# Performance work log

Hardware: AMD Instinct MI355X
Metric: run time of the kernel (lower is better)

The kernel has to match this reference:

```python
import jax, jax.numpy as jnp
import numpy as np

B, S, D = 8, 4096, 1024
C = D // 4          # bottleneck width (downsize=4)
P = 64              # num_prompt_tokens
EPS = 1e-5          # BatchNorm1d eps


def setup_inputs() -> dict:
    key = jax.random.key(0)
    ks = jax.random.split(key, 5)
    return {
        "hidden_states": jax.random.normal(ks[0], (B, S, D), dtype=jnp.float32),
        "W_down": jax.random.normal(ks[1], (C, D), dtype=jnp.float32) / np.sqrt(D),
        "b_down": jax.random.normal(ks[2], (C,), dtype=jnp.float32) * 0.02,
        "gamma": jnp.ones((C,), dtype=jnp.float32),
        "beta": jnp.zeros((C,), dtype=jnp.float32),
        "W_up": jax.random.normal(ks[3], (D, C), dtype=jnp.float32) / np.sqrt(C),
        "b_up": jax.random.normal(ks[4], (D,), dtype=jnp.float32) * 0.02,
    }


def reference(hidden_states, W_down, b_down, gamma, beta, W_up, b_up):
    # proj_down: [B,S,D] -> [B,S,C]
    h = jnp.einsum("bsd,cd->bsc", hidden_states, W_down) + b_down
    b, s, c = h.shape
    win = s // P  # S is a multiple of P, so AdaptiveMaxPool1d == windowed max
    # adaptive max pool over the sequence dim: [B,S,C] -> [B,P,C]
    h = h.reshape(b, P, win, c).max(axis=2)
    h = jax.nn.relu(h)
    # BatchNorm1d over channel dim (training mode: batch stats over B and P)
    mean = h.mean(axis=(0, 1))
    var = ((h - mean) ** 2).mean(axis=(0, 1))  # biased variance, as in BN
    h = (h - mean) * jax.lax.rsqrt(var + EPS) * gamma + beta
    # proj_up: [B,P,C] -> [B,P,D]
    return jnp.einsum("bpc,dc->bpd", h, W_up) + b_up
```

## Files before the change

kernel.cpp:

```cpp
#include <hip/hip_runtime.h>

#define D_  1024
#define C_  256
#define NBP 512

using bf16x8 = __attribute__((ext_vector_type(8))) __bf16;
using f32x4  = __attribute__((ext_vector_type(4))) float;

__device__ __forceinline__ unsigned short f2bf(float x) {
  unsigned int u = __float_as_uint(x);
  u += 0x7fffu + ((u >> 16) & 1u);
  return (unsigned short)(u >> 16);
}

typedef __attribute__((address_space(1))) const void* gas_t;
typedef __attribute__((address_space(3))) void* las_t;
__device__ __forceinline__ void dma16(const void* g, void* l) {
  __builtin_amdgcn_global_load_lds((gas_t)g, (las_t)l, 16, 0, 0);
}

__global__ void k_prep(const float* __restrict__ wdown, const float* __restrict__ wup,
                       unsigned short* __restrict__ wdb, float* __restrict__ wupT,
                       float* __restrict__ gsum, float* __restrict__ gsq) {
  int bid = blockIdx.x, tid = threadIdx.x;
  if (bid < 256) {
    int idx = (bid * 256 + tid) * 4;
    float4 v = *(const float4*)(wdown + idx);
    int ch = idx >> 10;
    int d  = idx & 1023;
    int kt = d >> 6;
    int c  = d & 63;
    ushort4 o;
    o.x = f2bf(v.x); o.y = f2bf(v.y); o.z = f2bf(v.z); o.w = f2bf(v.w);
    int dstbyte = kt * 32768 + ch * 128 + ((c * 2) ^ ((ch & 7) << 4));
    *(ushort4*)((char*)wdb + dstbyte) = o;
  } else if (bid < 320) {
    __shared__ float t[64][68];
    int b2 = bid - 256;
    int d0 = (b2 >> 2) * 64, c0 = (b2 & 3) * 64;
    #pragma unroll
    for (int r = 0; r < 4; ++r) {
      int idx = r * 256 + tid;
      int dr = idx >> 4, c4 = idx & 15;
      float4 v = *(const float4*)(wup + (d0 + dr) * C_ + c0 + c4 * 4);
      t[dr][c4*4+0] = v.x; t[dr][c4*4+1] = v.y; t[dr][c4*4+2] = v.z; t[dr][c4*4+3] = v.w;
    }
    __syncthreads();
    #pragma unroll
    for (int r = 0; r < 4; ++r) {
      int idx = r * 256 + tid;
      int cr = idx >> 4, d4 = idx & 15;
      float4 v;
      v.x = t[d4*4+0][cr]; v.y = t[d4*4+1][cr]; v.z = t[d4*4+2][cr]; v.w = t[d4*4+3][cr];
      *(float4*)(wupT + (c0 + cr) * D_ + d0 + d4 * 4) = v;
    }
  } else {
    gsum[tid] = 0.f;
    gsq[tid]  = 0.f;
  }
}

__global__ __launch_bounds__(256, 2)
void k_down_pool(const float* __restrict__ hid, const unsigned short* __restrict__ wdb,
                 const float* __restrict__ bdown, float* __restrict__ pooled,
                 float* __restrict__ gsum, float* __restrict__ gsq) {
  __shared__ unsigned short sA0[4096], sA1[4096];
  __shared__ unsigned short sB0[16384], sB1[16384];
  const int bp   = blockIdx.x;
  const int tid  = threadIdx.x;
  const int lane = tid & 63;
  const int wv   = tid >> 6;
  const int l15  = lane & 15;
  const int lg   = lane >> 4;

  const float* hbase = hid + (size_t)bp * 64 * D_;

  f32x4 acc[4][4] = {};
  float4 areg[4];

  auto issueB = [&](unsigned short* sB, int kt) {
    const char* src = (const char*)wdb + kt * 32768;
    #pragma unroll
    for (int i = 0; i < 8; ++i) {
      int off = (i * 4 + wv) * 1024 + lane * 16;
      dma16(src + off, (char*)sB + off);
    }
  };
  auto loadA = [&](int kt) {
    #pragma unroll
    for (int i = 0; i < 4; ++i) {
      int idx = i * 256 + tid;
      int row = idx >> 4, c4 = idx & 15;
      areg[i] = *(const float4*)(hbase + row * D_ + kt * 64 + c4 * 4);
    }
  };
  auto writeA = [&](unsigned short* sA) {
    #pragma unroll
    for (int i = 0; i < 4; ++i) {
      int idx = i * 256 + tid;
      int row = idx >> 4, c4 = idx & 15;
      ushort4 h;
      h.x = f2bf(areg[i].x); h.y = f2bf(areg[i].y); h.z = f2bf(areg[i].z); h.w = f2bf(areg[i].w);
      int off = row * 128 + ((c4 * 8) ^ ((row & 7) << 4));
      *(ushort4*)((char*)sA + off) = h;
    }
  };
  auto compute = [&](const unsigned short* sA, const unsigned short* sB) {
    #pragma unroll
    for (int ks = 0; ks < 2; ++ks) {
      bf16x8 afr[4], bfr[4];
      #pragma unroll
      for (int m = 0; m < 4; ++m) {
        int row = m * 16 + l15;
        int off = row * 128 + ((ks * 64 + lg * 16) ^ ((row & 7) << 4));
        union { uint4 u; bf16x8 v; } t;
        t.u = *(const uint4*)((const char*)sA + off);
        afr[m] = t.v;
      }
      #pragma unroll
      for (int n = 0; n < 4; ++n) {
        int row = wv * 64 + n * 16 + l15;
        int off = row * 128 + ((ks * 64 + lg * 16) ^ ((row & 7) << 4));
        union { uint4 u; bf16x8 v; } t;
        t.u = *(const uint4*)((const char*)sB + off);
        bfr[n] = t.v;
      }
      #pragma unroll
      for (int m = 0; m < 4; ++m)
        #pragma unroll
        for (int n = 0; n < 4; ++n)
          acc[m][n] = __builtin_amdgcn_mfma_f32_16x16x32_bf16(afr[m], bfr[n], acc[m][n], 0, 0, 0);
    }
  };

  issueB(sB0, 0);
  loadA(0);
  writeA(sA0);
  __syncthreads();

  #pragma unroll 1
  for (int kt = 0; kt < 16; kt += 2) {
    issueB(sB1, kt + 1);
    loadA(kt + 1);
    compute(sA0, sB0);
    writeA(sA1);
    __syncthreads();
    if (kt + 2 < 16) {
      issueB(sB0, kt + 2);
      loadA(kt + 2);
    }
    compute(sA1, sB1);
    if (kt + 2 < 16) writeA(sA0);
    __syncthreads();
  }

  #pragma unroll
  for (int n = 0; n < 4; ++n) {
    float vmax = -__builtin_inff();
    #pragma unroll
    for (int m = 0; m < 4; ++m)
      #pragma unroll
      for (int r = 0; r < 4; ++r)
        vmax = fmaxf(vmax, acc[m][n][r]);
    vmax = fmaxf(vmax, __shfl_xor(vmax, 16, 64));
    vmax = fmaxf(vmax, __shfl_xor(vmax, 32, 64));
    int col = wv * 64 + n * 16 + l15;
    if (lane < 16) {
      float pv = fmaxf(vmax + bdown[col], 0.f);
      pooled[bp * C_ + col] = pv;
      atomicAdd(&gsum[col], pv);
      atomicAdd(&gsq[col],  pv * pv);
    }
  }
}

__global__ void k_stats_final(const float* __restrict__ gsum, const float* __restrict__ gsq,
                              const float* __restrict__ gamma, const float* __restrict__ beta,
                              float* __restrict__ scale, float* __restrict__ shift) {
  int c = threadIdx.x;
  float mean = gsum[c] * (1.f / 512.f);
  float var  = gsq[c] * (1.f / 512.f) - mean * mean;
  float inv  = 1.f / sqrtf(var + 1e-5f);
  float sc = gamma[c] * inv;
  scale[c] = sc;
  shift[c] = beta[c] - mean * sc;
}

__global__ __launch_bounds__(256)
void k_up(const float* __restrict__ pooled, const float* __restrict__ wupT,
          const float* __restrict__ scale, const float* __restrict__ shift,
          const float* __restrict__ bup, float* __restrict__ out) {
  __shared__ float sx0[256], sx1[256];
  int tid = threadIdx.x;
  int r0 = blockIdx.x * 2;
  float sc = scale[tid], sh = shift[tid];
  sx0[tid] = pooled[r0 * C_ + tid] * sc + sh;
  sx1[tid] = pooled[(r0 + 1) * C_ + tid] * sc + sh;
  __syncthreads();
  int d4 = tid * 4;
  float a0=0,a1=0,a2=0,a3=0,b0=0,b1=0,b2=0,b3=0;
  #pragma unroll 8
  for (int k = 0; k < 256; ++k) {
    float4 w = *(const float4*)(wupT + (size_t)k * D_ + d4);
    float x0 = sx0[k], x1 = sx1[k];
    a0 += w.x * x0; a1 += w.y * x0; a2 += w.z * x0; a3 += w.w * x0;
    b0 += w.x * x1; b1 += w.y * x1; b2 += w.z * x1; b3 += w.w * x1;
  }
  float4 bb = *(const float4*)(bup + d4);
  float4 o0 = {a0 + bb.x, a1 + bb.y, a2 + bb.z, a3 + bb.w};
  float4 o1 = {b0 + bb.x, b1 + bb.y, b2 + bb.z, b3 + bb.w};
  *(float4*)(out + (size_t)r0 * D_ + d4) = o0;
  *(float4*)(out + (size_t)(r0 + 1) * D_ + d4) = o1;
}

extern "C" void kernel_launch(void* const* d_in, const int* in_sizes, int n_in,
                              void* d_out, int out_size, void* d_ws, size_t ws_size,
                              hipStream_t stream) {
  const float* hid   = (const float*)d_in[0];
  const float* wdown = (const float*)d_in[1];
  const float* bdown = (const float*)d_in[2];
  const float* gamma = (const float*)d_in[3];
  const float* beta  = (const float*)d_in[4];
  const float* wup   = (const float*)d_in[5];
  const float* bup   = (const float*)d_in[6];
  float* out = (float*)d_out;

  char* ws = (char*)d_ws;
  unsigned short* wdb = (unsigned short*)ws;
  float* wupT   = (float*)(ws + (512 << 10));
  float* pooled = (float*)(ws + (1536 << 10));
  float* gsum   = (float*)(ws + (2048 << 10));
  float* gsq    = (float*)(ws + (2048 << 10) + 1024);
  float* scale  = (float*)(ws + (2048 << 10) + 2048);
  float* shiftv = (float*)(ws + (2048 << 10) + 3072);

  hipLaunchKernelGGL(k_prep,        dim3(321), dim3(256), 0, stream, wdown, wup, wdb, wupT, gsum, gsq);
  hipLaunchKernelGGL(k_down_pool,   dim3(512), dim3(256), 0, stream, hid, wdb, bdown, pooled, gsum, gsq);
  hipLaunchKernelGGL(k_stats_final, dim3(1),   dim3(256), 0, stream, gsum, gsq, gamma, beta, scale, shiftv);
  hipLaunchKernelGGL(k_up,          dim3(256), dim3(256), 0, stream, pooled, wupT, scale, shiftv, bup, out);
}
```

Measured before the change: 238.2 us.

## Pipeline down-projection loads with explicit waitcnts and fold BN finalize into up kernel

Restructures the GEMM main loop in k_down_pool. It issues the A and B global loads for step i+2 right after the barrier and uses explicit s_waitcnt vmcnt counts plus raw s_barrier instead of __syncthreads, so memory latency overlaps the MFMA compute further ahead. It also removes the single-block k_stats_final launch by having every k_up block recompute scale and shift from gsum and gsq. The trade-off is fragile hand-counted wait values that depend on the compiler's instruction ordering, plus a small amount of redundant per-block arithmetic.

```diff
diff --git a/kernel.cpp b/kernel.cpp
--- a/kernel.cpp
+++ b/kernel.cpp
@@ -2,7 +2,6 @@
 
 #define D_  1024
 #define C_  256
-#define NBP 512
 
 using bf16x8 = __attribute__((ext_vector_type(8))) __bf16;
 using f32x4  = __attribute__((ext_vector_type(4))) float;
@@ -133,25 +132,45 @@
     }
   };
 
+  loadA(0);
+  __builtin_amdgcn_sched_barrier(0);
   issueB(sB0, 0);
-  loadA(0);
+  __builtin_amdgcn_sched_barrier(0);
+  asm volatile("s_waitcnt vmcnt(8)" ::: "memory");
   writeA(sA0);
-  __syncthreads();
+  __builtin_amdgcn_sched_barrier(0);
+  loadA(1);
+  __builtin_amdgcn_sched_barrier(0);
+  issueB(sB1, 1);
+  __builtin_amdgcn_sched_barrier(0);
+  asm volatile("s_waitcnt vmcnt(12) lgkmcnt(0)" ::: "memory");
+  __builtin_amdgcn_s_barrier();
+
+  auto step = [&](int i, unsigned short* curA, unsigned short* curB,
+                  unsigned short* nxtA, unsigned short* nxtB) {
+    compute(curA, curB);
+    if (i + 1 < 16) {
+      asm volatile("s_waitcnt vmcnt(8)" ::: "memory");
+      writeA(nxtA);
+    }
+    asm volatile("s_waitcnt lgkmcnt(0)" ::: "memory");
+    __builtin_amdgcn_s_barrier();
+    if (i + 2 < 16) {
+      loadA(i + 2);
+      __builtin_amdgcn_sched_barrier(0);
+      issueB(curB, i + 2);
+      __builtin_amdgcn_sched_barrier(0);
+      asm volatile("s_waitcnt vmcnt(12)" ::: "memory");
+    } else {
+      asm volatile("s_waitcnt vmcnt(0)" ::: "memory");
+    }
+    __builtin_amdgcn_s_barrier();
+  };
 
   #pragma unroll 1
   for (int kt = 0; kt < 16; kt += 2) {
-    issueB(sB1, kt + 1);
-    loadA(kt + 1);
-    compute(sA0, sB0);
-    writeA(sA1);
-    __syncthreads();
-    if (kt + 2 < 16) {
-      issueB(sB0, kt + 2);
-      loadA(kt + 2);
-    }
-    compute(sA1, sB1);
-    if (kt + 2 < 16) writeA(sA0);
-    __syncthreads();
+    step(kt,     sA0, sB0, sA1, sB1);
+    step(kt + 1, sA1, sB1, sA0, sB0);
   }
 
   #pragma unroll
@@ -174,26 +193,19 @@
   }
 }
 
-__global__ void k_stats_final(const float* __restrict__ gsum, const float* __restrict__ gsq,
-                              const float* __restrict__ gamma, const float* __restrict__ beta,
-                              float* __restrict__ scale, float* __restrict__ shift) {
-  int c = threadIdx.x;
-  float mean = gsum[c] * (1.f / 512.f);
-  float var  = gsq[c] * (1.f / 512.f) - mean * mean;
-  float inv  = 1.f / sqrtf(var + 1e-5f);
-  float sc = gamma[c] * inv;
-  scale[c] = sc;
-  shift[c] = beta[c] - mean * sc;
-}
-
 __global__ __launch_bounds__(256)
 void k_up(const float* __restrict__ pooled, const float* __restrict__ wupT,
-          const float* __restrict__ scale, const float* __restrict__ shift,
+          const float* __restrict__ gsum, const float* __restrict__ gsq,
+          const float* __restrict__ gamma, const float* __restrict__ beta,
           const float* __restrict__ bup, float* __restrict__ out) {
   __shared__ float sx0[256], sx1[256];
   int tid = threadIdx.x;
   int r0 = blockIdx.x * 2;
-  float sc = scale[tid], sh = shift[tid];
+  float mean = gsum[tid] * (1.f / 512.f);
+  float var  = gsq[tid] * (1.f / 512.f) - mean * mean;
+  float inv  = 1.f / sqrtf(var + 1e-5f);
+  float sc = gamma[tid] * inv;
+  float sh = beta[tid] - mean * sc;
   sx0[tid] = pooled[r0 * C_ + tid] * sc + sh;
   sx1[tid] = pooled[(r0 + 1) * C_ + tid] * sc + sh;
   __syncthreads();
@@ -231,11 +243,8 @@
   float* pooled = (float*)(ws + (1536 << 10));
   float* gsum   = (float*)(ws + (2048 << 10));
   float* gsq    = (float*)(ws + (2048 << 10) + 1024);
-  float* scale  = (float*)(ws + (2048 << 10) + 2048);
-  float* shiftv = (float*)(ws + (2048 << 10) + 3072);
-
-  hipLaunchKernelGGL(k_prep,        dim3(321), dim3(256), 0, stream, wdown, wup, wdb, wupT, gsum, gsq);
-  hipLaunchKernelGGL(k_down_pool,   dim3(512), dim3(256), 0, stream, hid, wdb, bdown, pooled, gsum, gsq);
-  hipLaunchKernelGGL(k_stats_final, dim3(1),   dim3(256), 0, stream, gsum, gsq, gamma, beta, scale, shiftv);
-  hipLaunchKernelGGL(k_up,          dim3(256), dim3(256), 0, stream, pooled, wupT, scale, shiftv, bup, out);
-}
+
+  hipLaunchKernelGGL(k_prep,      dim3(321), dim3(256), 0, stream, wdown, wup, wdb, wupT, gsum, gsq);
+  hipLaunchKernelGGL(k_down_pool, dim3(512), dim3(256), 0, stream, hid, wdb, bdown, pooled, gsum, gsq);
+  hipLaunchKernelGGL(k_up,        dim3(256), dim3(256), 0, stream, pooled, wupT, gsum, gsq, gamma, beta, bup, out);
+}
```

Result: no change. 240.3 us (+0.9%).
